# Kernel optimization log

Hardware: AMD Instinct MI355X
Metric: run time of the kernel (lower is better)

## Reference

```python
import jax, jax.numpy as jnp
import numpy as np
from jax import lax

B, H, W = 2, 960, 1280
K = 1024            # max_keypoints
P = 256             # num_pairs (BAD descriptor dim)
NUM_SCALES = 3
DIFF_ITERS = 3
KAPPA = 0.05
TAU = 0.2           # explicit FED step size (stable < 0.25)
DET_THRESHOLD = 0.001
AKAZE_NMS = 5       # detector-internal NMS window
NMS_WIN = 2 * 3 + 1 # pipeline NMS window (nms_radius=3)
ORI_PATCH = 15
ORI_SIGMA = 2.5
SINK_ITERS = 20
EPSILON = 1.0
UNUSED_SCORE = 1.0
MAX_RADIUS = 5

def _conv(x, k):
    return lax.conv_general_dilated(x, k, (1, 1), 'SAME', dimension_numbers=('NCHW', 'OIHW', 'NCHW'))

_sob = np.array([[-1., 0., 1.], [-2., 0., 2.], [-1., 0., 1.]], np.float32) / 8.0
KX = jnp.asarray(_sob)[None, None]
KY = jnp.asarray(_sob.T)[None, None]
_d2 = np.array([[0., 0., 0.], [1., -2., 1.], [0., 0., 0.]], np.float32)
KXX = jnp.asarray(_d2)[None, None]
KYY = jnp.asarray(_d2.T)[None, None]

# Gaussian weighting kernel for orientation estimation
_c = np.arange(ORI_PATCH, dtype=np.float32) - (ORI_PATCH - 1) / 2.0
_gy, _gx = np.meshgrid(_c, _c, indexing='ij')
_g = np.exp(-(_gx ** 2 + _gy ** 2) / (2.0 * ORI_SIGMA ** 2))
GK = jnp.asarray((_g / _g.sum()).astype(np.float32))[None, None]

# Box-average kernel bank: one normalized box filter per radius 0..MAX_RADIUS
_bc = np.arange(-MAX_RADIUS, MAX_RADIUS + 1, dtype=np.float32)
_by, _bx = np.meshgrid(_bc, _bc, indexing='ij')
_rv = np.arange(MAX_RADIUS + 1, dtype=np.float32)[:, None, None]
_bm = ((np.abs(_by) <= _rv) & (np.abs(_bx) <= _rv)).astype(np.float32)
BOX_BANK = jnp.asarray((_bm / (2.0 * _rv + 1.0) ** 2)[:, None])  # [R+1,1,11,11]

def _shifts(a):
    p = jnp.pad(a, ((0, 0), (0, 0), (1, 1), (1, 1)), mode='edge')
    return p[:, :, :-2, 1:-1], p[:, :, 2:, 1:-1], p[:, :, 1:-1, :-2], p[:, :, 1:-1, 2:]

def _fed_step(L):
    # One explicit Perona-Malik (FED) nonlinear diffusion step
    Lx = _conv(L, KX); Ly = _conv(L, KY)
    g = 1.0 / (1.0 + (Lx * Lx + Ly * Ly) / (KAPPA * KAPPA))
    Ln, Ls, Lw, Le = _shifts(L)
    gn, gs, gw, ge = _shifts(g)
    flux = 0.5 * ((g + gn) * (Ln - L) + (g + gs) * (Ls - L) + (g + gw) * (Lw - L) + (g + ge) * (Le - L))
    return L + TAU * flux

def _maxpool(s, win):
    return lax.reduce_window(s, -jnp.inf, lax.max, (1, win, win), (1, 1, 1), 'SAME')

def _akaze(img):
    # Multi-scale FED diffusion -> Hessian determinant response + orientation map
    L = img
    resp = jnp.zeros((B, H, W), img.dtype)
    for _s in range(NUM_SCALES):
        for _i in range(DIFF_ITERS):
            L = _fed_step(L)
        Lxx = _conv(L, KXX); Lyy = _conv(L, KYY); Lxy = _conv(_conv(L, KX), KY)
        resp = jnp.maximum(resp, (Lxx * Lyy - Lxy * Lxy)[:, 0])
    resp = jnp.where(resp > DET_THRESHOLD, resp, 0.0)
    resp = resp * (resp >= _maxpool(resp, AKAZE_NMS) - 1e-7).astype(resp.dtype)
    gxs = _conv(_conv(img, KX), GK)[:, 0]
    gys = _conv(_conv(img, KY), GK)[:, 0]
    theta = jnp.arctan2(gys, gxs)  # [B,H,W]
    return resp, theta

def _select(resp):
    # Pipeline-level maxpool NMS + top-K selection, pad invalid with (-1,-1)
    mask = (resp >= _maxpool(resp, NMS_WIN) - 1e-7).astype(resp.dtype)
    s = resp * mask
    s = jnp.where(s > 0.0, s, 0.0)
    tk, idx = lax.top_k(s.reshape(B, -1), K)
    y = (idx // W).astype(jnp.float32)
    x = (idx % W).astype(jnp.float32)
    valid = (tk > 0.0).astype(jnp.float32)
    kpts = jnp.where(valid[..., None] > 0.5, jnp.stack([y, x], -1), -1.0)
    return kpts, tk * valid, valid

def _bad(img, kpts, theta, valid, offsets, radii, thresholds):
    # Orientation-aware BAD: box-averaged intensity differences at rotated pair offsets
    bank = _conv(img, BOX_BANK)  # [B,R+1,H,W]
    yc = jnp.clip(kpts[..., 0], 0.0, H - 1.0)
    xc = jnp.clip(kpts[..., 1], 0.0, W - 1.0)
    yi = jnp.round(yc).astype(jnp.int32); xi = jnp.round(xc).astype(jnp.int32)
    th = jax.vmap(lambda m, a, b: m[a, b])(theta, yi, xi)  # [B,K] nearest-sampled orientation
    c = jnp.cos(th)[..., None]; s = jnp.sin(th)[..., None]
    ox1, oy1, ox2, oy2 = offsets[:, 0], offsets[:, 1], offsets[:, 2], offsets[:, 3]
    px1 = xc[..., None] + c * ox1 - s * oy1
    py1 = yc[..., None] + s * ox1 + c * oy1
    px2 = xc[..., None] + c * ox2 - s * oy2
    py2 = yc[..., None] + s * ox2 + c * oy2
    rb = jnp.broadcast_to(radii[None, :], (K, P))
    def samp(px, py):
        xi_ = jnp.clip(jnp.round(px), 0, W - 1).astype(jnp.int32)
        yi_ = jnp.clip(jnp.round(py), 0, H - 1).astype(jnp.int32)
        return jax.vmap(lambda bk, a, b: bk[rb, a, b])(bank, yi_, xi_)  # [B,K,P]
    v = (samp(px1, py1) - samp(px2, py2)) - thresholds[None, None, :]
    v = v * valid[..., None]
    n = jnp.linalg.norm(v, axis=-1, keepdims=True)
    return v / (n + 1e-8)

def _sinkhorn(d1, d2):
    sq1 = jnp.sum(d1 * d1, -1); sq2 = jnp.sum(d2 * d2, -1)
    dist2 = sq1[:, :, None] + sq2[:, None, :] - 2.0 * jnp.einsum('bip,bjp->bij', d1, d2)
    dist = jnp.sqrt(jnp.maximum(dist2, 0.0) + 1e-12)
    Z = jnp.full((B, K + 1, K + 1), UNUSED_SCORE, d1.dtype)
    Z = Z.at[:, :K, :K].set(-dist) / EPSILON
    norm = -jnp.log(2.0 * K)
    log_mu = jnp.concatenate([jnp.zeros(K, Z.dtype), jnp.log(float(K)) * jnp.ones(1, Z.dtype)]) + norm
    log_nu = log_mu
    def body(carry, _):
        u, v = carry
        u = log_mu[None] - jax.nn.logsumexp(Z + v[:, None, :], axis=2)
        v = log_nu[None] - jax.nn.logsumexp(Z + u[:, :, None], axis=1)
        return (u, v), None
    (u, v), _ = lax.scan(body, (jnp.zeros((B, K + 1), Z.dtype), jnp.zeros((B, K + 1), Z.dtype)), None, length=SINK_ITERS)
    return jnp.exp(Z + u[:, :, None] + v[:, None, :] - norm)  # [B,K+1,K+1]

def _forward(img1, img2, offsets, thresholds, radii):
    r1, t1 = _akaze(img1)
    r2, t2 = _akaze(img2)
    k1, s1, v1 = _select(r1)
    k2, s2, v2 = _select(r2)
    d1 = _bad(img1, k1, t1, v1, offsets, radii, thresholds)
    d2 = _bad(img2, k2, t2, v2, offsets, radii, thresholds)
    probs = _sinkhorn(d1, d2)
    return k1, k2, probs

def setup_inputs():
    key = jax.random.key(0)
    k1, k2, k3, k4, k5 = jax.random.split(key, 5)
    img1 = jax.random.uniform(k1, (B, 1, H, W), jnp.float32)
    img2 = jax.random.uniform(k2, (B, 1, H, W), jnp.float32)
    offsets = jax.random.uniform(k3, (P, 4), jnp.float32, -16.0, 16.0)  # box_params - 16
    thresholds = 0.05 * jax.random.normal(k5, (P,), jnp.float32)
    radii = jax.random.randint(k4, (P,), 0, MAX_RADIUS + 1, jnp.int32)
    return {'img1': img1, 'img2': img2, 'offsets': offsets, 'thresholds': thresholds, 'radii': radii}

def reference(img1, img2, offsets, thresholds, radii):
    return _forward(img1, img2, offsets, thresholds, radii)
```

## Files before the change

kernel.cpp:

```cpp
#include <hip/hip_runtime.h>
#include <hip/hip_fp16.h>
#include <math.h>

typedef unsigned long long u64;
typedef unsigned int u32;

#define Hh 960
#define Ww 1280
#define Bb 2
#define Kk 1024
#define Pp 256
#define KP1 1025
#define NSEG 4
#define LISTCAP 131072
#define PR 28
#define PS 57
#define ZLD 1040
#define CANDCAP 8192
#define KEYCAP 256
static const size_t ZB = (size_t)KP1*ZLD;

static const size_t HWp = (size_t)Hh * Ww;
static const size_t PLn = HWp * Bb;

#define TAUf 0.2f
#define NMS_EPS 1e-7f
#define DET_T 0.001f
#define NORMV (-7.6246189861593985f)
#define LOGKV (6.9314718055994531f)

__constant__ float WR[6] = {1.0f, 1.0f/9.0f, 1.0f/25.0f, 1.0f/49.0f, 1.0f/81.0f, 1.0f/121.0f};

__device__ __forceinline__ int imin(int a,int b){return a<b?a:b;}
__device__ __forceinline__ int imax(int a,int b){return a>b?a:b;}

__device__ __forceinline__ float4 ld4z(const float* __restrict__ S, int gy, int gxq){
  float4 v;
  if(gy>=0&&gy<Hh&&gxq>=0&&gxq+3<Ww){
    v=*reinterpret_cast<const float4*>(&S[(size_t)gy*Ww+gxq]);
  }else{
    v.x=(gy>=0&&gy<Hh&&gxq>=0&&gxq<Ww)?S[(size_t)gy*Ww+gxq]:0.0f;
    v.y=(gy>=0&&gy<Hh&&gxq+1>=0&&gxq+1<Ww)?S[(size_t)gy*Ww+gxq+1]:0.0f;
    v.z=(gy>=0&&gy<Hh&&gxq+2>=0&&gxq+2<Ww)?S[(size_t)gy*Ww+gxq+2]:0.0f;
    v.w=(gy>=0&&gy<Hh&&gxq+3>=0&&gxq+3<Ww)?S[(size_t)gy*Ww+gxq+3]:0.0f;
  }
  return v;
}

__global__ __launch_bounds__(256) void fed2_step(const float* __restrict__ src, float* __restrict__ dst,
                const float* __restrict__ img1, const float* __restrict__ img2, int fromImgs){
  __shared__ float Lt[40][41];
  __shared__ float Gt[38][39];
  __shared__ float Lp[36][37];
  const int bx=blockIdx.x*32, by=blockIdx.y*32, b=blockIdx.z;
  const int gx0=bx-4, gy0=by-4;
  const float* S = fromImgs ? ((b<2?img1:img2)+(size_t)(b&1)*HWp) : (src+(size_t)b*HWp);
  float* D=dst+(size_t)b*HWp;
  const int t=threadIdx.y*32+threadIdx.x;
  const float k2=(float)(0.05*0.05);
  for(int i=t;i<40*10;i+=256){
    int ly=i/10, q=i-(i/10)*10;
    float4 v=ld4z(S, gy0+ly, gx0+q*4);
    int lx=q*4;
    Lt[ly][lx]=v.x; Lt[ly][lx+1]=v.y; Lt[ly][lx+2]=v.z; Lt[ly][lx+3]=v.w;
  }
  __syncthreads();
  for(int i=t;i<38*38;i+=256){
    int y=i/38+1, x=i-(i/38)*38+1;
    float sx=(-Lt[y-1][x-1]+Lt[y-1][x+1]-2.0f*Lt[y][x-1]+2.0f*Lt[y][x+1]-Lt[y+1][x-1]+Lt[y+1][x+1])*0.125f;
    float sy=(-Lt[y-1][x-1]-2.0f*Lt[y-1][x]-Lt[y-1][x+1]+Lt[y+1][x-1]+2.0f*Lt[y+1][x]+Lt[y+1][x+1])*0.125f;
    Gt[y-1][x-1]=1.0f/(1.0f+(sx*sx+sy*sy)/k2);
  }
  __syncthreads();
  for(int i=t;i<36*36;i+=256){
    int y=i/36+2, x=i-(i/36)*36+2;
    int gy=gy0+y, gx=gx0+x;
    float v=0.0f;
    if(gy>=0&&gy<Hh&&gx>=0&&gx<Ww){
      int yn=imax(gy-1,0)-gy0, ys=imin(gy+1,Hh-1)-gy0;
      int xw=imax(gx-1,0)-gx0, xe=imin(gx+1,Ww-1)-gx0;
      float Lc=Lt[y][x];
      float Ln=Lt[yn][x], Ls=Lt[ys][x], Lw=Lt[y][xw], Le=Lt[y][xe];
      float gc=Gt[y-1][x-1], gn=Gt[yn-1][x-1], gs=Gt[ys-1][x-1], gw=Gt[y-1][xw-1], ge=Gt[y-1][xe-1];
      float flux=0.5f*((gc+gn)*(Ln-Lc)+(gc+gs)*(Ls-Lc)+(gc+gw)*(Lw-Lc)+(gc+ge)*(Le-Lc));
      v=Lc+TAUf*flux;
    }
    Lp[y-2][x-2]=v;
  }
  __syncthreads();
  for(int i=t;i<34*34;i+=256){
    int y=i/34+1, x=i-(i/34)*34+1;
    float sx=(-Lp[y-1][x-1]+Lp[y-1][x+1]-2.0f*Lp[y][x-1]+2.0f*Lp[y][x+1]-Lp[y+1][x-1]+Lp[y+1][x+1])*0.125f;
    float sy=(-Lp[y-1][x-1]-2.0f*Lp[y-1][x]-Lp[y-1][x+1]+Lp[y+1][x-1]+2.0f*Lp[y+1][x]+Lp[y+1][x+1])*0.125f;
    Gt[y-1][x-1]=1.0f/(1.0f+(sx*sx+sy*sy)/k2);
  }
  __syncthreads();
  for(int i=t;i<32*8;i+=256){
    int oy=i>>3, ox4=(i&7)<<2;
    float vals[4];
    #pragma unroll
    for(int kq=0;kq<4;kq++){
      int ox=ox4+kq;
      int y=oy+2, x=ox+2;
      int gy=by+oy, gx=bx+ox;
      int yn=imax(gy-1,0)-(gy0+2), ys=imin(gy+1,Hh-1)-(gy0+2);
      int xw=imax(gx-1,0)-(gx0+2), xe=imin(gx+1,Ww-1)-(gx0+2);
      float Lc=Lp[y][x];
      float Ln=Lp[yn][x], Ls=Lp[ys][x], Lw=Lp[y][xw], Le=Lp[y][xe];
      float gc=Gt[y-1][x-1], gn=Gt[yn-1][x-1], gs=Gt[ys-1][x-1], gw=Gt[y-1][xw-1], ge=Gt[y-1][xe-1];
      float flux=0.5f*((gc+gn)*(Ln-Lc)+(gc+gs)*(Ls-Lc)+(gc+gw)*(Lw-Lc)+(gc+ge)*(Le-Lc));
      vals[kq]=Lc+TAUf*flux;
    }
    float4 o; o.x=vals[0]; o.y=vals[1]; o.z=vals[2]; o.w=vals[3];
    *reinterpret_cast<float4*>(&D[(size_t)(by+oy)*Ww+bx+ox4])=o;
  }
}

__global__ __launch_bounds__(256) void fed_step_resp(const float* __restrict__ src, float* __restrict__ dstL,
                                                     float* __restrict__ resp, int first){
  __shared__ float Lt[40][41];
  __shared__ float Gt[38][39];
  __shared__ float Lp[36][37];
  const int bx=blockIdx.x*32, by=blockIdx.y*32, b=blockIdx.z;
  const int gx0=bx-4, gy0=by-4;
  const float* S=src+(size_t)b*HWp;
  float* DL=dstL+(size_t)b*HWp;
  float* R=resp+(size_t)b*HWp;
  const int t=threadIdx.y*32+threadIdx.x;
  const float k2=(float)(0.05*0.05);
  for(int i=t;i<40*10;i+=256){
    int ly=i/10, q=i-(i/10)*10;
    float4 v=ld4z(S, gy0+ly, gx0+q*4);
    int lx=q*4;
    Lt[ly][lx]=v.x; Lt[ly][lx+1]=v.y; Lt[ly][lx+2]=v.z; Lt[ly][lx+3]=v.w;
  }
  __syncthreads();
  for(int i=t;i<38*38;i+=256){
    int y=i/38+1, x=i-(i/38)*38+1;
    float sx=(-Lt[y-1][x-1]+Lt[y-1][x+1]
              -2.0f*Lt[y][x-1]+2.0f*Lt[y][x+1]
              -Lt[y+1][x-1]+Lt[y+1][x+1])*0.125f;
    float sy=(-Lt[y-1][x-1]-2.0f*Lt[y-1][x]-Lt[y-1][x+1]
              +Lt[y+1][x-1]+2.0f*Lt[y+1][x]+Lt[y+1][x+1])*0.125f;
    Gt[y-1][x-1]=1.0f/(1.0f+(sx*sx+sy*sy)/k2);
  }
  __syncthreads();
  for(int i=t;i<36*36;i+=256){
    int y=i/36+2, x=i-(i/36)*36+2;
    int gy=gy0+y, gx=gx0+x;
    float v=0.0f;
    if(gy>=0&&gy<Hh&&gx>=0&&gx<Ww){
      int yn=imax(gy-1,0)-gy0, ys=imin(gy+1,Hh-1)-gy0;
      int xw=imax(gx-1,0)-gx0, xe=imin(gx+1,Ww-1)-gx0;
      float Lc=Lt[y][x];
      float Ln=Lt[yn][x], Ls=Lt[ys][x], Lw=Lt[y][xw], Le=Lt[y][xe];
      float gc=Gt[y-1][x-1], gn=Gt[yn-1][x-1], gs=Gt[ys-1][x-1], gw=Gt[y-1][xw-1], ge=Gt[y-1][xe-1];
      float flux=0.5f*((gc+gn)*(Ln-Lc)+(gc+gs)*(Ls-Lc)+(gc+gw)*(Lw-Lc)+(gc+ge)*(Le-Lc));
      v=Lc+TAUf*flux;
    }
    Lp[y-2][x-2]=v;
  }
  __syncthreads();
  for(int i=t;i<32*8;i+=256){
    int oy=i>>3, ox4=(i&7)<<2;
    float4 o;
    o.x=Lp[oy+2][ox4+2]; o.y=Lp[oy+2][ox4+3]; o.z=Lp[oy+2][ox4+4]; o.w=Lp[oy+2][ox4+5];
    *reinterpret_cast<float4*>(&DL[(size_t)(by+oy)*Ww+bx+ox4])=o;
  }
  for(int i=t;i<34*34;i+=256){
    int y=i/34+1, x=i-(i/34)*34+1;
    int gy=gy0+2+y, gx=gx0+2+x;
    float v=0.0f;
    if(gy>=0&&gy<Hh&&gx>=0&&gx<Ww){
      v=(-Lp[y-1][x-1]+Lp[y-1][x+1]
         -2.0f*Lp[y][x-1]+2.0f*Lp[y][x+1]
         -Lp[y+1][x-1]+Lp[y+1][x+1])*0.125f;
    }
    Gt[y-1][x-1]=v;
  }
  __syncthreads();
  for(int i=t;i<32*8;i+=256){
    int oy=i>>3, ox4=(i&7)<<2;
    float* rp=&R[(size_t)(by+oy)*Ww+bx+ox4];
    float4 rv;
    if(!first) rv=*reinterpret_cast<const float4*>(rp);
    float dets[4];
    #pragma unroll
    for(int kq=0;kq<4;kq++){
      int y=oy+2, x=ox4+kq+2;
      float Lxx=Lp[y][x-1]-2.0f*Lp[y][x]+Lp[y][x+1];
      float Lyy=Lp[y-1][x]-2.0f*Lp[y][x]+Lp[y+1][x];
      float Lxy=(-Gt[y-2][x-2]-2.0f*Gt[y-2][x-1]-Gt[y-2][x]
                 +Gt[y][x-2]+2.0f*Gt[y][x-1]+Gt[y][x])*0.125f;
      dets[kq]=Lxx*Lyy-Lxy*Lxy;
    }
    float4 o;
    o.x=first?fmaxf(dets[0],0.0f):fmaxf(rv.x,dets[0]);
    o.y=first?fmaxf(dets[1],0.0f):fmaxf(rv.y,dets[1]);
    o.z=first?fmaxf(dets[2],0.0f):fmaxf(rv.z,dets[2]);
    o.w=first?fmaxf(dets[3],0.0f):fmaxf(rv.w,dets[3]);
    *reinterpret_cast<float4*>(rp)=o;
  }
}

__global__ __launch_bounds__(256) void detect_compact(const float* __restrict__ resp,
                                                      u64* __restrict__ lists,
                                                      int* __restrict__ cnt, int segbase){
  __shared__ float Tt[42][49];
  __shared__ u64 bm[38];
  __shared__ u64 keys[KEYCAP];
  __shared__ int lcnt, gbase;
  const int bx = blockIdx.x*32, by = blockIdx.y*32, b = blockIdx.z;
  const float* S = resp + (size_t)b*HWp;
  const int t = threadIdx.y*32 + threadIdx.x;
  if (t==0) lcnt=0;
  for (int i=t;i<42*12;i+=256){
    int ly=i/12, q=i-(i/12)*12;
    float4 v=ld4z(S, by+ly-5, bx-8+q*4);
    int lx=q*4;
    Tt[ly][lx  ]=(v.x>DET_T)?v.x:0.0f;
    Tt[ly][lx+1]=(v.y>DET_T)?v.y:0.0f;
    Tt[ly][lx+2]=(v.z>DET_T)?v.z:0.0f;
    Tt[ly][lx+3]=(v.w>DET_T)?v.w:0.0f;
  }
  __syncthreads();
  {
    int wave=t>>6, lane=t&63;
    for(int y=wave; y<38; y+=4){
      bool pred=false;
      if(lane<38){
        float m=0.0f;
        #pragma unroll
        for(int dy=0;dy<5;dy++)
          #pragma unroll
          for(int dx=0;dx<5;dx++)
            m=fmaxf(m,Tt[y+dy][lane+3+dx]);
        float c=Tt[y+2][lane+5];
        pred=(c>0.0f)&&(c>=m-NMS_EPS);
      }
      u64 mask=__ballot(pred);
      if(lane==0) bm[y]=mask;
    }
  }
  __syncthreads();
  const int seg=segbase+b;
  for (int r=0;r<4;++r){
    int oy=threadIdx.y + r*8, ox=threadIdx.x;
    bool pos=false; u64 key=0;
    if((bm[oy+3]>>(ox+3))&1ULL){
      float v=Tt[oy+5][ox+8];
      float m=0.0f;
      #pragma unroll
      for(int dy=0;dy<7;dy++){
        u32 chunk=(u32)((bm[oy+dy]>>ox)&0x7FULL);
        while(chunk){
          int j=__ffs(chunk)-1;
          m=fmaxf(m,Tt[oy+dy+2][ox+j+5]);
          chunk&=chunk-1;
        }
      }
      if(v>=m-NMS_EPS){
        u32 idx=(u32)((by+oy)*Ww+(bx+ox));
        key=((u64)__float_as_uint(v)<<32)|(u64)(0xFFFFFFFFu-idx);
        pos=true;
      }
    }
    u64 mask=__ballot(pos);
    if (mask){
      int lane=t&63;
      int leader=__ffsll((long long)mask)-1;
      int base=0;
      if (lane==leader) base=atomicAdd(&lcnt,__popcll(mask));
      base=__shfl(base,leader);
      if (pos){
        int rk=__popcll(mask & ((1ULL<<lane)-1ULL));
        if(base+rk<KEYCAP) keys[base+rk]=key;
      }
    }
  }
  __syncthreads();
  int n=imin(lcnt,KEYCAP);
  if (t==0 && n>0) gbase=atomicAdd(&cnt[seg*64], n);
  __syncthreads();
  for (int i=t;i<n;i+=256){
    int p=gbase+i;
    if (p<LISTCAP) lists[(size_t)seg*LISTCAP+p]=keys[i];
  }
}

__global__ __launch_bounds__(256) void topk_hist16(const u64* __restrict__ lists, const int* __restrict__ cnt,
                                                   u32* __restrict__ h16){
  int seg=blockIdx.y;
  int n=imin(cnt[seg*64],LISTCAP);
  const u64* L=lists+(size_t)seg*LISTCAP;
  u32* H=h16+(size_t)seg*65536;
  for(int i=blockIdx.x*256+threadIdx.x;i<n;i+=gridDim.x*256){
    u32 b=(u32)(L[i]>>48);
    atomicAdd(&H[b],1u);
  }
}

__global__ __launch_bounds__(1024) void topk_decide16(const u32* __restrict__ h16, const int* __restrict__ cnt,
                                                      int* __restrict__ b16o, int* __restrict__ krem16,
                                                      int* __restrict__ takeAll, u64* __restrict__ Tf){
  int seg=blockIdx.x, tid=threadIdx.x;
  __shared__ u32 sc[1024];
  const u32* H=h16+(size_t)seg*65536;
  int n=imin(cnt[seg*64],LISTCAP);
  if(n<=Kk){
    if(tid==0){ takeAll[seg]=1; Tf[seg]=1ULL; b16o[seg]=-1; }
    return;
  }
  u32 csum=0;
  u32 hl[64];
  #pragma unroll 8
  for(int j=0;j<64;j++){ hl[j]=H[tid*64+j]; csum+=hl[j]; }
  sc[tid]=csum;
  __syncthreads();
  for(int off=1;off<1024;off<<=1){
    u32 v=(tid+off<1024)?sc[tid+off]:0u;
    __syncthreads();
    sc[tid]+=v;
    __syncthreads();
  }
  u32 nxt=(tid<1023)?sc[tid+1]:0u;
  if(sc[tid]>=(u32)Kk && nxt<(u32)Kk){
    u32 run=nxt;
    for(int j=63;j>=0;j--){
      u32 c=hl[j];
      run+=c;
      if(run>=(u32)Kk){
        b16o[seg]=tid*64+j;
        krem16[seg]=Kk-(int)(run-c);
        takeAll[seg]=0;
        break;
      }
    }
  }
}

__global__ __launch_bounds__(256) void topk_compact(const u64* __restrict__ lists, const int* __restrict__ cnt,
                                                    const int* __restrict__ b16o, const int* __restrict__ takeAll,
                                                    u64* __restrict__ candbuf, int* __restrict__ candcnt){
  int seg=blockIdx.y;
  if(takeAll[seg]) return;
  int n=imin(cnt[seg*64],LISTCAP);
  const u64* L=lists+(size_t)seg*LISTCAP;
  u32 b16=(u32)b16o[seg];
  for(int i0=blockIdx.x*256;i0<n;i0+=gridDim.x*256){
    int i=i0+threadIdx.x;
    bool sel=false; u64 k=0;
    if(i<n){ k=L[i]; sel=((u32)(k>>48)==b16); }
    u64 mask=__ballot(sel);
    if(mask){
      int lane=threadIdx.x&63;
      int leader=__ffsll((long long)mask)-1;
      int base=0;
      if(lane==leader) base=atomicAdd(&candcnt[seg*64],__popcll(mask));
      base=__shfl(base,leader);
      if(sel){
        int p=base+__popcll(mask & ((1ULL<<lane)-1ULL));
        if(p<CANDCAP) candbuf[(size_t)seg*CANDCAP+p]=k;
      }
    }
  }
}

__global__ __launch_bounds__(1024) void topk_finish(const u64* __restrict__ lists, const int* __restrict__ cnt,
                                                    const u64* __restrict__ candbuf, const int* __restrict__ candcnt,
                                                    const int* __restrict__ b16o, const int* __restrict__ krem16,
                                                    const int* __restrict__ takeAll, u64* __restrict__ Tf){
  int seg=blockIdx.x, tid=threadIdx.x;
  if(takeAll[seg]) return;
  __shared__ u64 cands[CANDCAP];
  __shared__ u32 h[256], scan[256];
  __shared__ int bsel;
  int cc=candcnt[seg*64];
  u64 pfx=((u64)(u32)b16o[seg])<<48;
  int kr=krem16[seg];
  if(cc<=CANDCAP){
    for(int i=tid;i<cc;i+=1024) cands[i]=candbuf[(size_t)seg*CANDCAP+i];
    __syncthreads();
    for(int rd=0;rd<6;rd++){
      int shift=40-8*rd;
      u64 maskHi=~0ULL<<(shift+8);
      if(tid<256) h[tid]=0;
      __syncthreads();
      for(int i=tid;i<cc;i+=1024){
        u64 k=cands[i];
        if((k&maskHi)==pfx) atomicAdd(&h[(int)((k>>shift)&255ULL)],1u);
      }
      __syncthreads();
      if(tid<256) scan[tid]=h[tid];
      __syncthreads();
      for(int off=1;off<256;off<<=1){
        u32 v=0;
        if(tid<256 && tid+off<256) v=scan[tid+off];
        __syncthreads();
        if(tid<256) scan[tid]+=v;
        __syncthreads();
      }
      if(tid<256){
        bool ge=(scan[tid]>=(u32)kr);
        bool geN=(tid<255)?(scan[tid+1]>=(u32)kr):false;
        if(ge && !geN) bsel=tid;
      }
      __syncthreads();
      int b=bsel;
      int acc=(b<255)?(int)scan[b+1]:0;
      pfx |= ((u64)(u32)b)<<shift;
      kr -= acc;
      __syncthreads();
    }
  } else {
    int n=imin(cnt[seg*64],LISTCAP);
    const u64* L=lists+(size_t)seg*LISTCAP;
    for(int rd=0;rd<6;rd++){
      int shift=40-8*rd;
      u64 maskHi=~0ULL<<(shift+8);
      if(tid<256) h[tid]=0;
      __syncthreads();
      for(int i=tid;i<n;i+=1024){
        u64 k=L[i];
        if((k&maskHi)==pfx) atomicAdd(&h[(int)((k>>shift)&255ULL)],1u);
      }
      __syncthreads();
      if(tid<256) scan[tid]=h[tid];
      __syncthreads();
      for(int off=1;off<256;off<<=1){
        u32 v=0;
        if(tid<256 && tid+off<256) v=scan[tid+off];
        __syncthreads();
        if(tid<256) scan[tid]+=v;
        __syncthreads();
      }
      if(tid<256){
        bool ge=(scan[tid]>=(u32)kr);
        bool geN=(tid<255)?(scan[tid+1]>=(u32)kr):false;
        if(ge && !geN) bsel=tid;
      }
      __syncthreads();
      int b=bsel;
      int acc=(b<255)?(int)scan[b+1]:0;
      pfx |= ((u64)(u32)b)<<shift;
      kr -= acc;
      __syncthreads();
    }
  }
  if(tid==0) Tf[seg]=pfx;
}

__global__ __launch_bounds__(256) void topk_gather(const u64* __restrict__ lists, const int* __restrict__ cnt,
                                                   const u64* __restrict__ Tf, u64* __restrict__ selbuf,
                                                   int* __restrict__ selcnt){
  int seg=blockIdx.y;
  int n=imin(cnt[seg*64],LISTCAP);
  u64 T=Tf[seg];
  const u64* L=lists+(size_t)seg*LISTCAP;
  for(int i0=blockIdx.x*256;i0<n;i0+=gridDim.x*256){
    int i=i0+threadIdx.x;
    bool sel=false; u64 k=0;
    if(i<n){ k=L[i]; sel=(k>=T); }
    u64 mask=__ballot(sel);
    if(mask){
      int lane=threadIdx.x&63;
      int leader=__ffsll((long long)mask)-1;
      int base=0;
      if(lane==leader) base=atomicAdd(&selcnt[seg*64],__popcll(mask));
      base=__shfl(base,leader);
      if(sel){
        int p=base+__popcll(mask & ((1ULL<<lane)-1ULL));
        if(p<Kk) selbuf[(size_t)seg*Kk+p]=k;
      }
    }
  }
}

__global__ __launch_bounds__(1024) void finalize_kernel(const u64* __restrict__ selbuf, const int* __restrict__ selcnt,
                                int* __restrict__ kyi, int* __restrict__ kxi, float* __restrict__ kval,
                                float* __restrict__ outp){
  int seg=blockIdx.x, tid=threadIdx.x;
  __shared__ u64 a[1024];
  int n=selcnt[seg*64]; if(n>Kk)n=Kk;
  a[tid]=(tid<n)?selbuf[(size_t)seg*Kk+tid]:0ULL;
  __syncthreads();
  for(int k=2;k<=1024;k<<=1){
    for(int j=k>>1;j>0;j>>=1){
      int ixj=tid^j;
      if(ixj>tid){
        u64 x=a[tid], y=a[ixj];
        bool desc=((tid&k)==0);
        if(desc ? (x<y) : (x>y)){ a[tid]=y; a[ixj]=x; }
      }
      __syncthreads();
    }
  }
  u64 key=a[tid];
  bool val=(key!=0ULL);
  u32 idx=0xFFFFFFFFu-(u32)(key&0xFFFFFFFFULL);
  int y= val ? (int)(idx/Ww) : 0;
  int x= val ? (int)(idx%Ww) : 0;
  int mi=seg*Kk+tid;
  kyi[mi]=y; kxi[mi]=x; kval[mi]= val?1.0f:0.0f;
  int imi=seg>>1, bb=seg&1;
  float* ko=outp + (size_t)imi*(Bb*Kk*2) + ((size_t)bb*Kk+tid)*2;
  ko[0]= val ? (float)y : -1.0f;
  ko[1]= val ? (float)x : -1.0f;
}

__global__ __launch_bounds__(256) void bad_kernel(const float* __restrict__ img1, const float* __restrict__ img2,
                           const float* __restrict__ offs, const float* __restrict__ thrv,
                           const int* __restrict__ rad,
                           const int* __restrict__ kyi, const int* __restrict__ kxi,
                           const float* __restrict__ kval,
                           float* __restrict__ d1, float* __restrict__ d2,
                           float* __restrict__ sq1, float* __restrict__ sq2){
  __shared__ float sat[PS+1][PS+2];
  __shared__ float sm[4], smx[4], smy[4];
  __shared__ float w15s[15];
  __shared__ float nsh, thsh;
  int seg=blockIdx.y, ki=blockIdx.x, p=threadIdx.x;
  const float* img=(seg<2?img1:img2)+(size_t)(seg&1)*HWp;
  int mi=seg*Kk+ki;
  int yci=kyi[mi], xci=kxi[mi];
  if(p==0){
    double w[15]; double Sw=0.0;
    for(int i=0;i<15;i++){ double c=(double)i-7.0; w[i]=exp(-(c*c)/(2.0*2.5*2.5)); Sw+=w[i]; }
    for(int i=0;i<15;i++) w15s[i]=(float)(w[i]/Sw);
  }
  for (int i=p;i<PS+1;i+=256){ sat[0][i]=0.0f; sat[i][0]=0.0f; }
  if (p==0) sat[0][PS]=0.0f;
  for (int i=p;i<PS*PS;i+=256){
    int ly=i/PS, lx=i-ly*PS;
    int gy=yci-PR+ly, gx=xci-PR+lx;
    sat[ly+1][lx+1]=(gy>=0&&gy<Hh&&gx>=0&&gx<Ww)?img[(size_t)gy*Ww+gx]:0.0f;
  }
  __syncthreads();
  {
    float ax=0.0f, ay=0.0f;
    if(p<225){
      int du=p/15-7, dv=p-(p/15)*15-7;
      int yy=yci+du, xx=xci+dv;
      if(yy>=0&&yy<Hh&&xx>=0&&xx<Ww){
        int ly=du+PR+1, lx=dv+PR+1;
        float p00=sat[ly-1][lx-1], p01=sat[ly-1][lx], p02=sat[ly-1][lx+1];
        float p10=sat[ly][lx-1],                       p12=sat[ly][lx+1];
        float p20=sat[ly+1][lx-1], p21=sat[ly+1][lx], p22=sat[ly+1][lx+1];
        float sx=(-p00+p02-2.0f*p10+2.0f*p12-p20+p22)*0.125f;
        float sy=(-p00-2.0f*p01-p02+p20+2.0f*p21+p22)*0.125f;
        float wgt=w15s[du+7]*w15s[dv+7];
        ax=wgt*sx; ay=wgt*sy;
      }
    }
    for(int o=32;o;o>>=1){ ax+=__shfl_down(ax,o); ay+=__shfl_down(ay,o); }
    if((p&63)==0){ smx[p>>6]=ax; smy[p>>6]=ay; }
    __syncthreads();
    if(p==0) thsh=atan2f(smy[0]+smy[1]+smy[2]+smy[3], smx[0]+smx[1]+smx[2]+smx[3]);
  }
  __syncthreads();
  if (p<PS){
    float run=0.0f;
    for(int x=1;x<=PS;x++){ run+=sat[p+1][x]; sat[p+1][x]=run; }
  }
  __syncthreads();
  if (p<PS){
    float run=0.0f;
    for(int y=1;y<=PS;y++){ run+=sat[y][p+1]; sat[y][p+1]=run; }
  }
  __syncthreads();
  float yc=(float)yci, xc=(float)xci;
  float th=thsh;
  float c=cosf(th), s=sinf(th);
  float ox1=offs[p*4+0], oy1=offs[p*4+1], ox2=offs[p*4+2], oy2=offs[p*4+3];
  int r=rad[p];
  float w=WR[r];
  float px1=xc+c*ox1-s*oy1, py1=yc+s*ox1+c*oy1;
  float px2=xc+c*ox2-s*oy2, py2=yc+s*ox2+c*oy2;
  auto boxl=[&](float px,float py,int r_)->float{
    float rx=rintf(px), ry=rintf(py);
    int xi=(int)fminf(fmaxf(rx,0.0f),(float)(Ww-1));
    int yi=(int)fminf(fmaxf(ry,0.0f),(float)(Hh-1));
    int lx=xi-(xci-PR), ly=yi-(yci-PR);
    int y2=ly+r_+1, y1=ly-r_, x2=lx+r_+1, x1=lx-r_;
    return sat[y2][x2]-sat[y1][x2]-sat[y2][x1]+sat[y1][x1];
  };
  float s1=boxl(px1,py1,r)*w;
  float s2=boxl(px2,py2,r)*w;
  float v=(s1-s2-thrv[p])*kval[mi];
  float t=v*v;
  for(int o=32;o;o>>=1) t+=__shfl_down(t,o);
  if((p&63)==0) sm[p>>6]=t;
  __syncthreads();
  if(p==0) nsh=sqrtf(sm[0]+sm[1]+sm[2]+sm[3]);
  __syncthreads();
  float dv=v/(nsh+1e-8f);
  float* dd=(seg<2?d1:d2);
  dd[((size_t)(seg&1)*Kk+ki)*Pp+p]=dv;
  float t2=dv*dv;
  for(int o=32;o;o>>=1) t2+=__shfl_down(t2,o);
  __syncthreads();
  if((p&63)==0) sm[p>>6]=t2;
  __syncthreads();
  if(p==0){ float* sq=(seg<2?sq1:sq2); sq[(size_t)(seg&1)*Kk+ki]=sm[0]+sm[1]+sm[2]+sm[3]; }
}

__global__ __launch_bounds__(256) void dist_kernel(const float* __restrict__ d1, const float* __restrict__ d2,
                            const float* __restrict__ sq1, const float* __restrict__ sq2,
                            float* __restrict__ Zm, float* __restrict__ Zt){
  int b=blockIdx.z;
  int i0=blockIdx.y*64, j0=blockIdx.x*64;
  int tid=threadIdx.x;
  int tx=tid&15, ty=tid>>4;
  __shared__ float Ast[64][68], Bst[64][68];
  const float* D1=d1+(size_t)b*Kk*Pp;
  const float* D2=d2+(size_t)b*Kk*Pp;
  float acc[4][4]={};
  for(int p0=0;p0<Pp;p0+=64){
    for(int i=tid;i<64*16;i+=256){
      int row=i>>4, c4=(i&15)<<2;
      float4 va=*reinterpret_cast<const float4*>(&D1[(size_t)(i0+row)*Pp+p0+c4]);
      float4 vb=*reinterpret_cast<const float4*>(&D2[(size_t)(j0+row)*Pp+p0+c4]);
      Ast[c4+0][row]=va.x; Ast[c4+1][row]=va.y; Ast[c4+2][row]=va.z; Ast[c4+3][row]=va.w;
      Bst[c4+0][row]=vb.x; Bst[c4+1][row]=vb.y; Bst[c4+2][row]=vb.z; Bst[c4+3][row]=vb.w;
    }
    __syncthreads();
    #pragma unroll 8
    for(int kk=0;kk<64;++kk){
      float4 av=*reinterpret_cast<const float4*>(&Ast[kk][ty*4]);
      float4 bv=*reinterpret_cast<const float4*>(&Bst[kk][tx*4]);
      acc[0][0]=fmaf(av.x,bv.x,acc[0][0]); acc[0][1]=fmaf(av.x,bv.y,acc[0][1]);
      acc[0][2]=fmaf(av.x,bv.z,acc[0][2]); acc[0][3]=fmaf(av.x,bv.w,acc[0][3]);
      acc[1][0]=fmaf(av.y,bv.x,acc[1][0]); acc[1][1]=fmaf(av.y,bv.y,acc[1][1]);
      acc[1][2]=fmaf(av.y,bv.z,acc[1][2]); acc[1][3]=fmaf(av.y,bv.w,acc[1][3]);
      acc[2][0]=fmaf(av.z,bv.x,acc[2][0]); acc[2][1]=fmaf(av.z,bv.y,acc[2][1]);
      acc[2][2]=fmaf(av.z,bv.z,acc[2][2]); acc[2][3]=fmaf(av.z,bv.w,acc[2][3]);
      acc[3][0]=fmaf(av.w,bv.x,acc[3][0]); acc[3][1]=fmaf(av.w,bv.y,acc[3][1]);
      acc[3][2]=fmaf(av.w,bv.z,acc[3][2]); acc[3][3]=fmaf(av.w,bv.w,acc[3][3]);
    }
    __syncthreads();
  }
  int gi=i0+ty*4, gj=j0+tx*4;
  float si[4], sj[4];
  #pragma unroll
  for(int i=0;i<4;i++){ si[i]=sq1[b*Kk+gi+i]; sj[i]=sq2[b*Kk+gj+i]; }
  #pragma unroll
  for(int i=0;i<4;i++){
    #pragma unroll
    for(int j=0;j<4;j++){
      float dd=si[i]+sj[j]-2.0f*acc[i][j];
      float dist=sqrtf(fmaxf(dd,0.0f)+1e-12f);
      Zm[(size_t)b*ZB+(size_t)(gi+i)*ZLD+(gj+j)]=-dist;
      Zt[(size_t)b*ZB+(size_t)(gj+j)*ZLD+(gi+i)]=-dist;
    }
  }
}

__global__ void expz_kernel(float* __restrict__ Zm, float* __restrict__ Zt,
                            __half* __restrict__ Em, __half* __restrict__ Et,
                            float* __restrict__ euv, float* __restrict__ evv){
  size_t q=(size_t)blockIdx.x*256+threadIdx.x;
  const size_t tot4=(size_t)Bb*ZB/4;
  if(q>=2*tot4){
    size_t r=q-2*tot4;
    if(r<(size_t)Bb*ZLD){
      int j=(int)(r%(size_t)ZLD);
      evv[r]=(j<KP1)?1.0f:0.0f;
      euv[r]=0.0f;
    }
    return;
  }
  float* src=(q<tot4)?Zm:Zt;
  __half* dst=(q<tot4)?Em:Et;
  size_t j=(q<tot4)?q:q-tot4;
  size_t jb=j%(ZB/4);
  int r=(int)(jb/(ZLD/4));
  int c0=(int)(jb%(ZLD/4))*4;
  float4 z=reinterpret_cast<const float4*>(src)[j];
  float zz[4]={z.x,z.y,z.z,z.w};
  float e[4];
  bool wb=false;
  #pragma unroll
  for(int k=0;k<4;k++){
    int c=c0+k;
    if(c>=KP1) e[k]=0.0f;
    else if(r==Kk||c==Kk){ zz[k]=1.0f; e[k]=expf(1.0f); wb=true; }
    else e[k]=expf(zz[k]);
  }
  if(wb){
    float4 zo; zo.x=zz[0]; zo.y=zz[1]; zo.z=zz[2]; zo.w=zz[3];
    reinterpret_cast<float4*>(src)[j]=zo;
  }
  __half2 a=__floats2half2_rn(e[0],e[1]);
  __half2 b2=__floats2half2_rn(e[2],e[3]);
  reinterpret_cast<__half2*>(dst)[2*j]=a;
  reinterpret_cast<__half2*>(dst)[2*j+1]=b2;
}

struct H4{ __half2 a, b; };
__global__ __launch_bounds__(256) void sink_gemv(const __half* __restrict__ E,
        const float* __restrict__ evin, float* __restrict__ euout, float* __restrict__ uout){
  int row=blockIdx.x*4+(threadIdx.x>>6);
  if(row>=Bb*KP1) return;
  int b=row/KP1, i=row-b*KP1;
  int lane=threadIdx.x&63;
  const H4* e4=reinterpret_cast<const H4*>(E+((size_t)b*KP1+i)*ZLD);
  const float4* v4=reinterpret_cast<const float4*>(evin+(size_t)b*ZLD);
  float s=0.0f;
  for(int j=lane;j<ZLD/4;j+=64){
    H4 e=e4[j]; float4 v=v4[j];
    float2 ea=__half22float2(e.a), eb=__half22float2(e.b);
    s=fmaf(ea.x,v.x,s); s=fmaf(ea.y,v.y,s);
    s=fmaf(eb.x,v.z,s); s=fmaf(eb.y,v.w,s);
  }
  for(int o=32;o;o>>=1) s+=__shfl_down(s,o);
  if(lane==0){
    float lm,elm;
    if(i<Kk){ lm=NORMV; elm=4.8828125e-4f; }
    else    { lm=LOGKV+NORMV; elm=0.5f; }
    euout[(size_t)b*ZLD+i]=elm/s;
    uout [(size_t)b*ZLD+i]=lm-logf(s);
  }
}

__global__ void probs_kernel(const float* __restrict__ Zm, const float* __restrict__ uu,
                             const float* __restrict__ vv, float* __restrict__ outp){
  size_t i=(size_t)blockIdx.x*256+threadIdx.x;
  const size_t tot=(size_t)Bb*KP1*KP1;
  if(i>=tot) return;
  size_t b=i/((size_t)KP1*KP1);
  size_t rem=i-b*(size_t)KP1*KP1;
  int rr=(int)(rem/KP1), cc=(int)(rem-(size_t)(rem/KP1)*KP1);
  outp[i]=expf(Zm[b*ZB+(size_t)rr*ZLD+cc]+uu[b*ZLD+rr]+vv[b*ZLD+cc]-NORMV);
}

extern "C" void kernel_launch(void* const* d_in, const int* in_sizes, int n_in,
                              void* d_out, int out_size, void* d_ws, size_t ws_size,
                              hipStream_t stream) {
  (void)in_sizes; (void)n_in; (void)out_size;
  const float* img1=(const float*)d_in[0];
  const float* img2=(const float*)d_in[1];
  const float* offs=(const float*)d_in[2];
  const float* thrv=(const float*)d_in[3];
  const int*   rad =(const int*)d_in[4];
  float* out=(float*)d_out;

  const bool batched = ws_size >= ((size_t)80<<20);
  const int NP = batched ? 4 : 2;
  const size_t PB = HWp*(size_t)NP*4;

  char* wp=(char*)d_ws;
  auto carve=[&](size_t bytes)->char*{ char* p=wp; wp += (bytes+255)&~(size_t)255; return p; };
  float* r0  =(float*)carve(PB);
  float* r1  =(float*)carve(PB);
  float* resp=(float*)carve(PB);
  u64*  lists=(u64*)carve((size_t)NSEG*LISTCAP*8);
  char* stateblk = carve(8192);
  int* cnt     =(int*)(stateblk);
  int* selcnt  =(int*)(stateblk+1024);
  int* b16o    =(int*)(stateblk+2048);
  int* krem16  =(int*)(stateblk+2112);
  int* takeAll =(int*)(stateblk+2176);
  u64* Tf      =(u64*)(stateblk+2240);
  int* candcnt =(int*)(stateblk+4096);
  u32* h16     =(u32*)carve((size_t)NSEG*65536*4);
  u64* candbuf =(u64*)carve((size_t)NSEG*CANDCAP*8);
  u64* selbuf  =(u64*)carve((size_t)NSEG*Kk*8);
  int* kyi     =(int*)carve((size_t)NSEG*Kk*4);
  int* kxi     =(int*)carve((size_t)NSEG*Kk*4);
  float* kval  =(float*)carve((size_t)NSEG*Kk*4);
  float* d1    =(float*)carve((size_t)Bb*Kk*Pp*4);
  float* d2    =(float*)carve((size_t)Bb*Kk*Pp*4);
  float* sq1   =(float*)carve((size_t)Bb*Kk*4);
  float* sq2   =(float*)carve((size_t)Bb*Kk*4);
  float* uvec  =(float*)carve((size_t)Bb*ZLD*4);
  float* vvec  =(float*)carve((size_t)Bb*ZLD*4);
  float* euvec =(float*)carve((size_t)Bb*ZLD*4);
  float* evvec =(float*)carve((size_t)Bb*ZLD*4);

  const size_t EBYTES = ((size_t)Bb*ZB*2 + 255)&~(size_t)255;
  __half* Em=(__half*)resp;
  __half* Et=(__half*)((char*)resp + EBYTES);

  hipMemsetAsync(stateblk, 0, 8192 + (size_t)NSEG*65536*4, stream);

  dim3 TB(32,8);
  if (batched){
    dim3 TG(Ww/32, Hh/32, 4);
    fed2_step    <<<TG,TB,0,stream>>>(r0, r1, img1, img2, 1);
    fed_step_resp<<<TG,TB,0,stream>>>(r1, r0, resp, 1);
    fed2_step    <<<TG,TB,0,stream>>>(r0, r1, img1, img2, 0);
    fed_step_resp<<<TG,TB,0,stream>>>(r1, r0, resp, 0);
    fed2_step    <<<TG,TB,0,stream>>>(r0, r1, img1, img2, 0);
    fed_step_resp<<<TG,TB,0,stream>>>(r1, r0, resp, 0);
    detect_compact<<<TG,TB,0,stream>>>(resp, lists, cnt, 0);
  } else {
    dim3 TG(Ww/32, Hh/32, Bb);
    for(int im=0; im<2; ++im){
      const float* srcimg = (im==0)? img1 : img2;
      hipMemcpyAsync(r0, srcimg, PLn*4, hipMemcpyDeviceToDevice, stream);
      fed2_step    <<<TG,TB,0,stream>>>(r0, r1, img1, img2, 0);
      fed_step_resp<<<TG,TB,0,stream>>>(r1, r0, resp, 1);
      fed2_step    <<<TG,TB,0,stream>>>(r0, r1, img1, img2, 0);
      fed_step_resp<<<TG,TB,0,stream>>>(r1, r0, resp, 0);
      fed2_step    <<<TG,TB,0,stream>>>(r0, r1, img1, img2, 0);
      fed_step_resp<<<TG,TB,0,stream>>>(r1, r0, resp, 0);
      detect_compact<<<TG,TB,0,stream>>>(resp, lists, cnt, im*2);
    }
  }

  topk_hist16 <<<dim3(32,NSEG),dim3(256),0,stream>>>(lists, cnt, h16);
  topk_decide16<<<dim3(NSEG),dim3(1024),0,stream>>>(h16, cnt, b16o, krem16, takeAll, Tf);
  topk_compact<<<dim3(32,NSEG),dim3(256),0,stream>>>(lists, cnt, b16o, takeAll, candbuf, candcnt);
  topk_finish <<<dim3(NSEG),dim3(1024),0,stream>>>(lists, cnt, candbuf, candcnt, b16o, krem16, takeAll, Tf);
  topk_gather <<<dim3(32,NSEG),dim3(256),0,stream>>>(lists, cnt, Tf, selbuf, selcnt);
  finalize_kernel<<<NSEG,1024,0,stream>>>(selbuf, selcnt, kyi, kxi, kval, out);
  bad_kernel<<<dim3(Kk,NSEG),dim3(256),0,stream>>>(img1, img2, offs, thrv, rad,
                                                   kyi, kxi, kval, d1, d2, sq1, sq2);

  float* Zm=r0; float* Zt=r1;
  dist_kernel<<<dim3(16,16,Bb),dim3(256),0,stream>>>(d1,d2,sq1,sq2,Zm,Zt);
  {
    size_t tot4=(size_t)Bb*ZB/4;
    size_t totThreads=2*tot4 + (size_t)Bb*ZLD;
    expz_kernel<<<dim3((u32)((totThreads+255)/256)),dim3(256),0,stream>>>(Zm,Zt,Em,Et,euvec,evvec);
  }
  for(int it=0; it<20; ++it){
    sink_gemv<<<dim3((Bb*KP1+3)/4),dim3(256),0,stream>>>(Em, evvec, euvec, uvec);
    sink_gemv<<<dim3((Bb*KP1+3)/4),dim3(256),0,stream>>>(Et, euvec, evvec, vvec);
  }
  size_t tot=(size_t)Bb*KP1*KP1;
  probs_kernel<<<dim3((u32)((tot+255)/256)),dim3(256),0,stream>>>(Zm, uvec, vvec, out + (size_t)2*Bb*Kk*2);
}
```

Baseline: 538.9 us.

## Fuse final FED step and response max into detection kernel

Merges the last fed_step_resp launch into the detect/compact kernel. Each block recomputes the FED step, Hessian determinant and running-max response for its tile plus a halo in shared memory, then does NMS and compaction directly. This removes one kernel launch and a full write and re-read of the response and diffused image planes. In exchange it adds redundant halo computation and much more shared memory per block, which may lower occupancy.

```diff
diff --git a/kernel.cpp b/kernel.cpp
--- a/kernel.cpp
+++ b/kernel.cpp
@@ -203,25 +203,90 @@
   }
 }
 
-__global__ __launch_bounds__(256) void detect_compact(const float* __restrict__ resp,
-                                                      u64* __restrict__ lists,
-                                                      int* __restrict__ cnt, int segbase){
-  __shared__ float Tt[42][49];
+__global__ __launch_bounds__(256) void fed_resp_detect(const float* __restrict__ src,
+                const float* __restrict__ resp, u64* __restrict__ lists,
+                int* __restrict__ cnt, int segbase){
+  __shared__ float Lt[50][57];
+  __shared__ float Gt[48][49];
+  __shared__ float Lp[46][47];
+  __shared__ float Ro[42][49];
   __shared__ u64 bm[38];
   __shared__ u64 keys[KEYCAP];
   __shared__ int lcnt, gbase;
-  const int bx = blockIdx.x*32, by = blockIdx.y*32, b = blockIdx.z;
-  const float* S = resp + (size_t)b*HWp;
-  const int t = threadIdx.y*32 + threadIdx.x;
-  if (t==0) lcnt=0;
-  for (int i=t;i<42*12;i+=256){
+  const int bx=blockIdx.x*32, by=blockIdx.y*32, b=blockIdx.z;
+  const float* S=src+(size_t)b*HWp;
+  const float* R=resp+(size_t)b*HWp;
+  const int t=threadIdx.y*32+threadIdx.x;
+  const float k2=(float)(0.05*0.05);
+  if(t==0) lcnt=0;
+  for(int i=t;i<50*14;i+=256){
+    int ly=i/14, q=i-(i/14)*14;
+    float4 v=ld4z(S, by-9+ly, bx-12+q*4);
+    int lx=q*4;
+    Lt[ly][lx]=v.x; Lt[ly][lx+1]=v.y; Lt[ly][lx+2]=v.z; Lt[ly][lx+3]=v.w;
+  }
+  for(int i=t;i<42*12;i+=256){
     int ly=i/12, q=i-(i/12)*12;
-    float4 v=ld4z(S, by+ly-5, bx-8+q*4);
+    float4 v=ld4z(R, by-5+ly, bx-8+q*4);
     int lx=q*4;
-    Tt[ly][lx  ]=(v.x>DET_T)?v.x:0.0f;
-    Tt[ly][lx+1]=(v.y>DET_T)?v.y:0.0f;
-    Tt[ly][lx+2]=(v.z>DET_T)?v.z:0.0f;
-    Tt[ly][lx+3]=(v.w>DET_T)?v.w:0.0f;
+    Ro[ly][lx]=v.x; Ro[ly][lx+1]=v.y; Ro[ly][lx+2]=v.z; Ro[ly][lx+3]=v.w;
+  }
+  __syncthreads();
+  for(int i=t;i<48*48;i+=256){
+    int yy=i/48, xx=i-(i/48)*48;
+    int y=yy+1, x=xx+4;
+    float sx=(-Lt[y-1][x-1]+Lt[y-1][x+1]-2.0f*Lt[y][x-1]+2.0f*Lt[y][x+1]-Lt[y+1][x-1]+Lt[y+1][x+1])*0.125f;
+    float sy=(-Lt[y-1][x-1]-2.0f*Lt[y-1][x]-Lt[y-1][x+1]+Lt[y+1][x-1]+2.0f*Lt[y+1][x]+Lt[y+1][x+1])*0.125f;
+    Gt[yy][xx]=1.0f/(1.0f+(sx*sx+sy*sy)/k2);
+  }
+  __syncthreads();
+  for(int i=t;i<46*46;i+=256){
+    int py=i/46, px=i-(i/46)*46;
+    int gy=by-7+py, gx=bx-7+px;
+    float v=0.0f;
+    if(gy>=0&&gy<Hh&&gx>=0&&gx<Ww){
+      int yn=imax(gy-1,0), ys=imin(gy+1,Hh-1);
+      int xw=imax(gx-1,0), xe=imin(gx+1,Ww-1);
+      int lty=gy-(by-9), ltx=gx-(bx-12);
+      int ltyn=yn-(by-9), ltys=ys-(by-9), ltxw=xw-(bx-12), ltxe=xe-(bx-12);
+      float Lc=Lt[lty][ltx];
+      float Ln=Lt[ltyn][ltx], Ls=Lt[ltys][ltx], Lw=Lt[lty][ltxw], Le=Lt[lty][ltxe];
+      int gty=gy-(by-8), gtx=gx-(bx-8);
+      int gtyn=yn-(by-8), gtys=ys-(by-8), gtxw=xw-(bx-8), gtxe=xe-(bx-8);
+      float gc=Gt[gty][gtx], gn=Gt[gtyn][gtx], gs=Gt[gtys][gtx], gw=Gt[gty][gtxw], ge=Gt[gty][gtxe];
+      float flux=0.5f*((gc+gn)*(Ln-Lc)+(gc+gs)*(Ls-Lc)+(gc+gw)*(Lw-Lc)+(gc+ge)*(Le-Lc));
+      v=Lc+TAUf*flux;
+    }
+    Lp[py][px]=v;
+  }
+  __syncthreads();
+  for(int i=t;i<44*44;i+=256){
+    int sy=i/44, sx=i-(i/44)*44;
+    int gy=by-6+sy, gx=bx-6+sx;
+    float v=0.0f;
+    if(gy>=0&&gy<Hh&&gx>=0&&gx<Ww){
+      int py=sy+1, px=sx+1;
+      v=(-Lp[py-1][px-1]+Lp[py-1][px+1]-2.0f*Lp[py][px-1]+2.0f*Lp[py][px+1]-Lp[py+1][px-1]+Lp[py+1][px+1])*0.125f;
+    }
+    Gt[sy][sx]=v;
+  }
+  __syncthreads();
+  float (*Tt)[57]=Lt;
+  for(int i=t;i<42*42;i+=256){
+    int ty=i/42, tx=i-(i/42)*42;
+    int gy=by-5+ty, gx=bx-5+tx;
+    float val=0.0f;
+    if(gy>=0&&gy<Hh&&gx>=0&&gx<Ww){
+      int py=ty+2, px=tx+2;
+      float Lxx=Lp[py][px-1]-2.0f*Lp[py][px]+Lp[py][px+1];
+      float Lyy=Lp[py-1][px]-2.0f*Lp[py][px]+Lp[py+1][px];
+      float Lxy=(-Gt[ty][tx]-2.0f*Gt[ty][tx+1]-Gt[ty][tx+2]
+                 +Gt[ty+2][tx]+2.0f*Gt[ty+2][tx+1]+Gt[ty+2][tx+2])*0.125f;
+      float det=Lxx*Lyy-Lxy*Lxy;
+      float r=fmaxf(Ro[ty][tx+3], det);
+      val=(r>DET_T)?r:0.0f;
+    }
+    Tt[ty][tx]=val;
   }
   __syncthreads();
   {
@@ -234,8 +299,8 @@
         for(int dy=0;dy<5;dy++)
           #pragma unroll
           for(int dx=0;dx<5;dx++)
-            m=fmaxf(m,Tt[y+dy][lane+3+dx]);
-        float c=Tt[y+2][lane+5];
+            m=fmaxf(m,Tt[y+dy][lane+dx]);
+        float c=Tt[y+2][lane+2];
         pred=(c>0.0f)&&(c>=m-NMS_EPS);
       }
       u64 mask=__ballot(pred);
@@ -248,14 +313,14 @@
     int oy=threadIdx.y + r*8, ox=threadIdx.x;
     bool pos=false; u64 key=0;
     if((bm[oy+3]>>(ox+3))&1ULL){
-      float v=Tt[oy+5][ox+8];
+      float v=Tt[oy+5][ox+5];
       float m=0.0f;
       #pragma unroll
       for(int dy=0;dy<7;dy++){
         u32 chunk=(u32)((bm[oy+dy]>>ox)&0x7FULL);
         while(chunk){
           int j=__ffs(chunk)-1;
-          m=fmaxf(m,Tt[oy+dy+2][ox+j+5]);
+          m=fmaxf(m,Tt[oy+dy+2][ox+j+2]);
           chunk&=chunk-1;
         }
       }
@@ -786,25 +851,23 @@
   dim3 TB(32,8);
   if (batched){
     dim3 TG(Ww/32, Hh/32, 4);
-    fed2_step    <<<TG,TB,0,stream>>>(r0, r1, img1, img2, 1);
-    fed_step_resp<<<TG,TB,0,stream>>>(r1, r0, resp, 1);
-    fed2_step    <<<TG,TB,0,stream>>>(r0, r1, img1, img2, 0);
-    fed_step_resp<<<TG,TB,0,stream>>>(r1, r0, resp, 0);
-    fed2_step    <<<TG,TB,0,stream>>>(r0, r1, img1, img2, 0);
-    fed_step_resp<<<TG,TB,0,stream>>>(r1, r0, resp, 0);
-    detect_compact<<<TG,TB,0,stream>>>(resp, lists, cnt, 0);
+    fed2_step     <<<TG,TB,0,stream>>>(r0, r1, img1, img2, 1);
+    fed_step_resp <<<TG,TB,0,stream>>>(r1, r0, resp, 1);
+    fed2_step     <<<TG,TB,0,stream>>>(r0, r1, img1, img2, 0);
+    fed_step_resp <<<TG,TB,0,stream>>>(r1, r0, resp, 0);
+    fed2_step     <<<TG,TB,0,stream>>>(r0, r1, img1, img2, 0);
+    fed_resp_detect<<<TG,TB,0,stream>>>(r1, resp, lists, cnt, 0);
   } else {
     dim3 TG(Ww/32, Hh/32, Bb);
     for(int im=0; im<2; ++im){
       const float* srcimg = (im==0)? img1 : img2;
       hipMemcpyAsync(r0, srcimg, PLn*4, hipMemcpyDeviceToDevice, stream);
-      fed2_step    <<<TG,TB,0,stream>>>(r0, r1, img1, img2, 0);
-      fed_step_resp<<<TG,TB,0,stream>>>(r1, r0, resp, 1);
-      fed2_step    <<<TG,TB,0,stream>>>(r0, r1, img1, img2, 0);
-      fed_step_resp<<<TG,TB,0,stream>>>(r1, r0, resp, 0);
-      fed2_step    <<<TG,TB,0,stream>>>(r0, r1, img1, img2, 0);
-      fed_step_resp<<<TG,TB,0,stream>>>(r1, r0, resp, 0);
-      detect_compact<<<TG,TB,0,stream>>>(resp, lists, cnt, im*2);
+      fed2_step     <<<TG,TB,0,stream>>>(r0, r1, img1, img2, 0);
+      fed_step_resp <<<TG,TB,0,stream>>>(r1, r0, resp, 1);
+      fed2_step     <<<TG,TB,0,stream>>>(r0, r1, img1, img2, 0);
+      fed_step_resp <<<TG,TB,0,stream>>>(r1, r0, resp, 0);
+      fed2_step     <<<TG,TB,0,stream>>>(r0, r1, img1, img2, 0);
+      fed_resp_detect<<<TG,TB,0,stream>>>(r1, resp, lists, cnt, im*2);
     }
   }
 
```

New measurement: 557.5 us. 3.4% more time.
